# Kernel optimization log

Measured on AMD Instinct MI355X. Metric: run time of the kernel, lower is better.

The kernel has to match this reference:

```python
import jax, jax.numpy as jnp
import numpy as np

N_FACTORS = 8
CHANNEL = 4096
EPS = 1e-8


def setup_inputs() -> dict:
    key = jax.random.key(0)
    disen_weight_att = jax.random.normal(key, (N_FACTORS, CHANNEL), dtype=jnp.float32)
    return {"disen_weight_att": disen_weight_att}


def reference(disen_weight_att):
    # Faithful vectorized version of Cul_cor(ind='distance') forward:
    # sum over i<j of DistanceCorrelation(w[i], w[j]).
    x = disen_weight_att                      # [F, C]
    F_, C = x.shape
    sq = x ** 2                               # [F, C]
    # pairwise squared distances per factor: sq_k + sq_l - 2*x_k*x_l  -> [F, C, C]
    d = sq[:, :, None] + sq[:, None, :] - 2.0 * x[:, :, None] * x[:, None, :]
    a = jnp.sqrt(jnp.maximum(d, 0.0) + EPS)   # [F, C, C] distance matrices
    # double centering (a is symmetric, but keep both means for fidelity)
    row_mean = a.mean(axis=2, keepdims=True)  # mean over dim=1 in torch (per row)
    col_mean = a.mean(axis=1, keepdims=True)  # mean over dim=0 in torch (per col)
    tot_mean = a.mean(axis=(1, 2), keepdims=True)
    A = a - col_mean - row_mean + tot_mean    # [F, C, C]
    # all pairwise Frobenius inner products in one GEMM
    Af = A.reshape(F_, C * C)                 # [F, C*C]
    S = (Af @ Af.T) / (C ** 2)                # [F, F]; S[i,j] = (A_i*A_j).sum()/C^2
    dcov = jnp.sqrt(jnp.maximum(S, 0.0) + EPS)
    diag = jnp.diagonal(dcov)                 # dcov_AA per factor
    ratio = dcov / jnp.sqrt(diag[:, None] * diag[None, :] + EPS)
    mask = jnp.triu(jnp.ones((F_, F_), dtype=x.dtype), k=1)  # i < j pairs
    cor = jnp.sum(ratio * mask)
    return cor
```

## Files before the change

### kernel.cpp

```cpp
#include <hip/hip_runtime.h>
#include <math.h>

#define F 8
#define C 4096
#define NPAIR 36
#define EPSF 1e-8f

#define QCH 128
#define NQC (C / QCH)
#define NPG 32
#define NBLK (NPG * NQC)
#define XSROW 132

#define NSB 128
#define SO 116

#define WS_PART (NQC * F * C)
#define WS_GP   (NBLK * 256)

typedef __attribute__((ext_vector_type(8))) short short8v;
typedef __attribute__((ext_vector_type(4))) float f32x4;

__device__ __forceinline__ float wave_reduce(float v) {
    #pragma unroll
    for (int off = 32; off > 0; off >>= 1) v += __shfl_down(v, off, 64);
    return v;
}

__global__ __launch_bounds__(256) void gramrs_kernel(const float* __restrict__ x,
                                                     float* __restrict__ part,
                                                     float* __restrict__ gpart) {
    __shared__ __align__(16) float xs[F * XSROW];
    __shared__ float red[4 * 256];
    const int tid  = threadIdx.x;
    const int lane = tid & 63;
    const int wave = tid >> 6;
    const int pg = blockIdx.x >> 5;
    const int qc = blockIdx.x & 31;
    const int Q0 = qc * QCH;

    {
        const int sf = tid >> 5, si = tid & 31;
        *(float4*)(xs + sf * XSROW + 4 * si) =
            *(const float4*)(x + sf * C + Q0 + 4 * si);
    }

    const int f  = lane & 7;
    const int b  = (lane >> 3) & 1;
    const int hi = (lane >> 4) & 1;
    const int qq = (lane >> 5) & 1;
    const int p0 = (pg * 4 + wave) * 32 + 16 * b + 8 * hi;

    float xp[8];
    *(float4*)&xp[0] = *(const float4*)(x + f * C + p0);
    *(float4*)&xp[4] = *(const float4*)(x + f * C + p0 + 4);

    f32x4 acc = {0.f, 0.f, 0.f, 0.f};
    float rs[8];
    #pragma unroll
    for (int j = 0; j < 8; ++j) rs[j] = 0.f;

    __syncthreads();

    const float* xrow = xs + f * XSROW + qq;
    #pragma unroll 4
    for (int s = 0; s < QCH / 2; ++s) {
        const float xq = xrow[2 * s];
        float d[8];
        #pragma unroll
        for (int j = 0; j < 8; ++j) {
            d[j] = xq - xp[j];
            rs[j] += __builtin_fabsf(d[j]);
        }
        union { unsigned u[4]; short8v v; } fr;
        #pragma unroll
        for (int t = 0; t < 4; ++t)
            asm("v_cvt_pk_bf16_f32 %0, abs(%1), abs(%2)"
                : "=v"(fr.u[t]) : "v"(d[2 * t]), "v"(d[2 * t + 1]));
        acc = __builtin_amdgcn_mfma_f32_16x16x32_bf16(fr.v, fr.v, acc, 0, 0, 0);
    }

    #pragma unroll
    for (int j = 0; j < 8; ++j) rs[j] += __shfl_xor(rs[j], 32, 64);
    if (qq == 0) {
        float* dst = part + (qc * F + f) * C + p0;
        *(float4*)dst       = make_float4(rs[0], rs[1], rs[2], rs[3]);
        *(float4*)(dst + 4) = make_float4(rs[4], rs[5], rs[6], rs[7]);
    }

    {
        const int col = lane & 15, r0 = (lane >> 4) * 4;
        #pragma unroll
        for (int r = 0; r < 4; ++r)
            red[wave * 256 + (r0 + r) * 16 + col] = acc[r];
    }
    __syncthreads();
    gpart[blockIdx.x * 256 + tid] =
        red[tid] + red[256 + tid] + red[512 + tid] + red[768 + tid];
}

__global__ __launch_bounds__(256) void sred_kernel(const float* __restrict__ part,
                                                   const float* __restrict__ gpart,
                                                   float* __restrict__ sout) {
    __shared__ float sp[8][F][32];
    const int tid = threadIdx.x;
    const int pi  = tid & 31;
    const int qg  = tid >> 5;
    const int b   = blockIdx.x;
    const int p   = b * 32 + pi;

    float acc[F];
    #pragma unroll
    for (int f = 0; f < F; ++f) acc[f] = 0.0f;
    #pragma unroll
    for (int q4 = 0; q4 < NQC / 8; ++q4) {
        const int qc = qg * (NQC / 8) + q4;
        #pragma unroll
        for (int f = 0; f < F; ++f) acc[f] += part[(qc * F + f) * C + p];
    }
    #pragma unroll
    for (int f = 0; f < F; ++f) sp[qg][f][pi] = acc[f];
    __syncthreads();

    if (tid < 64) {
        float vals[44];
        if (tid < 32) {
            float sv[F];
            #pragma unroll
            for (int f = 0; f < F; ++f) {
                float s = 0.f;
                #pragma unroll
                for (int g2 = 0; g2 < 8; ++g2) s += sp[g2][f][pi];
                sv[f] = s;
            }
            int k = 0;
            #pragma unroll
            for (int i = 0; i < F; ++i)
                #pragma unroll
                for (int j = i; j < F; ++j) { vals[k] = sv[i] * sv[j]; ++k; }
            #pragma unroll
            for (int f2 = 0; f2 < F; ++f2) vals[36 + f2] = sv[f2];
        } else {
            #pragma unroll
            for (int k = 0; k < 44; ++k) vals[k] = 0.f;
        }
        #pragma unroll
        for (int k = 0; k < 44; ++k) vals[k] = wave_reduce(vals[k]);
        if (tid == 0) {
            #pragma unroll
            for (int k = 0; k < 44; ++k) sout[b * SO + k] = vals[k];
        }
    } else if (tid < 64 + 72) {
        const int e  = tid - 64;
        const int eb = (e >= 36) ? e - 36 : e;
        int i = 0, j = eb;
        while (j >= F - i) { j -= F - i; ++i; }
        j += i;
        const int ci = (e >= 36) ? (8 + i) * 16 + (8 + j) : i * 16 + j;
        float s = 0.f;
        #pragma unroll
        for (int r = 0; r < 8; ++r) s += gpart[(b * 8 + r) * 256 + ci];
        sout[b * SO + 44 + e] = s;
    }
}

__global__ __launch_bounds__(256) void finish_kernel(const float* __restrict__ sout,
                                                     float* __restrict__ out) {
    __shared__ float fA[SO][2];
    __shared__ float A[SO];
    const int tid = threadIdx.x;
    if (tid < SO * 2) {
        const int colx = tid >> 1, h = tid & 1;
        float s = 0.f;
        #pragma unroll 16
        for (int i = 0; i < NSB / 2; ++i)
            s += sout[(h * (NSB / 2) + i) * SO + colx];
        fA[colx][h] = s;
    }
    __syncthreads();
    if (tid < SO) A[tid] = fA[tid][0] + fA[tid][1];
    __syncthreads();
    if (tid == 0) {
        const float invC  = 1.0f / (float)C;
        const float invC2 = invC * invC;
        float dcov[NPAIR], diag[F];
        int k = 0;
        for (int i = 0; i < F; ++i)
            for (int j = i; j < F; ++j) {
                const float G = A[44 + k] + A[80 + k];
                const float S = G * invC2 - 2.0f * A[k] * invC2 * invC
                              + (A[36 + i] * invC2) * (A[36 + j] * invC2);
                const float dc = __builtin_amdgcn_sqrtf(fmaxf(S, 0.0f) + EPSF);
                dcov[k] = dc;
                if (i == j) diag[i] = dc;
                ++k;
            }
        float cor = 0.f;
        k = 0;
        for (int i = 0; i < F; ++i)
            for (int j = i; j < F; ++j) {
                if (j > i)
                    cor += dcov[k] * __builtin_amdgcn_rcpf(
                               __builtin_amdgcn_sqrtf(diag[i] * diag[j] + EPSF));
                ++k;
            }
        out[0] = cor;
    }
}

extern "C" void kernel_launch(void* const* d_in, const int* in_sizes, int n_in,
                              void* d_out, int out_size, void* d_ws, size_t ws_size,
                              hipStream_t stream) {
    const float* x = (const float*)d_in[0];
    float* part  = (float*)d_ws;
    float* gpart = part + WS_PART;
    float* sout  = gpart + WS_GP;
    float* out   = (float*)d_out;

    hipLaunchKernelGGL(gramrs_kernel, dim3(NBLK), dim3(256), 0, stream, x, part, gpart);
    hipLaunchKernelGGL(sred_kernel,   dim3(NSB),  dim3(256), 0, stream, part, gpart, sout);
    hipLaunchKernelGGL(finish_kernel, dim3(1),    dim3(256), 0, stream, sout, out);
}
```

Measured before the change: 76.60 us.

## Compute row sums via indicator-matrix MFMA and vectorize LDS reads

Replaces the per-lane VALU accumulation of absolute differences with a second MFMA against a constant bf16 indicator matrix, so the row sums come out of the matrix core. It also loads four q values at once with float4 LDS reads, giving each half-wave a contiguous 64-element range instead of interleaved scalar loads. This cuts VALU adds and removes the cross-lane shuffle reduction, at the cost of doubling MFMA issue and computing row sums from bf16-rounded values, which lowers their precision.

Result: faster. 70.67 us (median of 2 runs) (-7.7%).

```diff
diff --git a/kernel.cpp b/kernel.cpp
--- a/kernel.cpp
+++ b/kernel.cpp
@@ -49,43 +49,58 @@
     const int b  = (lane >> 3) & 1;
     const int hi = (lane >> 4) & 1;
     const int qq = (lane >> 5) & 1;
-    const int p0 = (pg * 4 + wave) * 32 + 16 * b + 8 * hi;
+    const int pgbase = (pg * 4 + wave) * 32;
+    const int p0 = pgbase + 16 * b + 8 * hi;
 
     float xp[8];
     *(float4*)&xp[0] = *(const float4*)(x + f * C + p0);
     *(float4*)&xp[4] = *(const float4*)(x + f * C + p0 + 4);
 
-    f32x4 acc = {0.f, 0.f, 0.f, 0.f};
-    float rs[8];
-    #pragma unroll
-    for (int j = 0; j < 8; ++j) rs[j] = 0.f;
-
-    __syncthreads();
-
-    const float* xrow = xs + f * XSROW + qq;
+    union { unsigned u[4]; short8v v; } ind;
+    {
+        const int col = lane & 15, gg = lane >> 4;
+        const int ea  = col - 8 * (gg & 1);
+        #pragma unroll
+        for (int t = 0; t < 4; ++t) {
+            const unsigned lo = (ea == 2 * t)     ? 0x3F80u : 0u;
+            const unsigned hb = (ea == 2 * t + 1) ? 0x3F80u : 0u;
+            ind.u[t] = lo | (hb << 16);
+        }
+    }
+
+    f32x4 acc    = {0.f, 0.f, 0.f, 0.f};
+    f32x4 acc_rs = {0.f, 0.f, 0.f, 0.f};
+
+    __syncthreads();
+
+    const float* xrow = xs + f * XSROW + 64 * qq;
     #pragma unroll 4
-    for (int s = 0; s < QCH / 2; ++s) {
-        const float xq = xrow[2 * s];
-        float d[8];
-        #pragma unroll
-        for (int j = 0; j < 8; ++j) {
-            d[j] = xq - xp[j];
-            rs[j] += __builtin_fabsf(d[j]);
-        }
-        union { unsigned u[4]; short8v v; } fr;
-        #pragma unroll
-        for (int t = 0; t < 4; ++t)
-            asm("v_cvt_pk_bf16_f32 %0, abs(%1), abs(%2)"
-                : "=v"(fr.u[t]) : "v"(d[2 * t]), "v"(d[2 * t + 1]));
-        acc = __builtin_amdgcn_mfma_f32_16x16x32_bf16(fr.v, fr.v, acc, 0, 0, 0);
-    }
-
-    #pragma unroll
-    for (int j = 0; j < 8; ++j) rs[j] += __shfl_xor(rs[j], 32, 64);
-    if (qq == 0) {
-        float* dst = part + (qc * F + f) * C + p0;
-        *(float4*)dst       = make_float4(rs[0], rs[1], rs[2], rs[3]);
-        *(float4*)(dst + 4) = make_float4(rs[4], rs[5], rs[6], rs[7]);
+    for (int s4 = 0; s4 < 16; ++s4) {
+        const float4 q4 = *(const float4*)(xrow + 4 * s4);
+        #pragma unroll
+        for (int u = 0; u < 4; ++u) {
+            const float xq = (u == 0) ? q4.x : (u == 1) ? q4.y : (u == 2) ? q4.z : q4.w;
+            float d[8];
+            #pragma unroll
+            for (int j = 0; j < 8; ++j) d[j] = xq - xp[j];
+            union { unsigned u32[4]; short8v v; } fr;
+            #pragma unroll
+            for (int t = 0; t < 4; ++t)
+                asm("v_cvt_pk_bf16_f32 %0, abs(%1), abs(%2)"
+                    : "=v"(fr.u32[t]) : "v"(d[2 * t]), "v"(d[2 * t + 1]));
+            acc    = __builtin_amdgcn_mfma_f32_16x16x32_bf16(fr.v, fr.v, acc, 0, 0, 0);
+            acc_rs = __builtin_amdgcn_mfma_f32_16x16x32_bf16(fr.v, ind.v, acc_rs, 0, 0, 0);
+        }
+    }
+
+    {
+        const int pslot = lane & 15;
+        #pragma unroll
+        for (int r = 0; r < 4; ++r) {
+            const int row = (lane >> 4) * 4 + r;
+            const int ff = row & 7, bb = row >> 3;
+            part[(qc * F + ff) * C + (pgbase + 16 * bb + pslot)] = acc_rs[r];
+        }
     }
 
     {
```
